# Performance work log

Hardware: AMD Instinct MI355X
Metric: run time of the kernel (lower is better)

Reference implementation:

```python
import jax, jax.numpy as jnp
import numpy as np

N_NODES = 50000
N_EDGES = 800000
N_GRAPHS = 2048


def setup_inputs() -> dict:
    key = jax.random.key(0)
    ks = jax.random.split(key, 16)
    x = jax.random.normal(ks[0], (N_NODES, 32), dtype=jnp.float32)
    edge_index = jax.random.randint(ks[1], (2, N_EDGES), 0, N_NODES, dtype=jnp.int64)
    batch = jnp.sort(jax.random.randint(ks[2], (N_NODES,), 0, N_GRAPHS, dtype=jnp.int64))
    def w(k, fi, fo):
        return jax.random.normal(k, (fi, fo), dtype=jnp.float32) * (1.0 / np.sqrt(fi))
    return {
        "x": x, "edge_index": edge_index, "batch": batch,
        "W1": w(ks[3], 32, 64), "b1": jnp.zeros((64,), jnp.float32),
        "W2": w(ks[4], 64, 64), "b2": jnp.zeros((64,), jnp.float32),
        "W3": w(ks[5], 64, 64), "b3": jnp.zeros((64,), jnp.float32),
        "lw1": w(ks[6], 64, 64), "lb1": jnp.zeros((64,), jnp.float32),
        "lw2": w(ks[7], 64, 2), "lb2": jnp.zeros((2,), jnp.float32),
    }


def reference(x, edge_index, batch, W1, b1, W2, b2, W3, b3, lw1, lb1, lw2, lb2):
    N = x.shape[0]
    # GCNConv default: add self loops, symmetric normalization
    loops = jnp.arange(N, dtype=edge_index.dtype)
    src = jnp.concatenate([edge_index[0], loops])
    dst = jnp.concatenate([edge_index[1], loops])
    ones = jnp.ones_like(src, dtype=x.dtype)
    deg = jax.ops.segment_sum(ones, dst, num_segments=N)  # in-degree incl. self loops
    dinv = jnp.where(deg > 0, jax.lax.rsqrt(deg), 0.0)
    norm = dinv[src] * dinv[dst]  # [E+N]

    def gcn_relu(h, W, b):
        h = h @ W                                    # [N, F]
        msg = h[src] * norm[:, None]                 # gather + scale [E+N, F]
        out = jax.ops.segment_sum(msg, dst, num_segments=N) + b
        return jax.nn.relu(out)

    h = gcn_relu(x, W1, b1)
    h = gcn_relu(h, W2, b2)
    h = gcn_relu(h, W3, b3)

    # global_mean_pool over graph ids
    summed = jax.ops.segment_sum(h, batch, num_segments=N_GRAPHS)  # [G, F]
    counts = jax.ops.segment_sum(jnp.ones((N,), h.dtype), batch, num_segments=N_GRAPHS)
    pooled = summed / jnp.maximum(counts, 1.0)[:, None]

    # dropout is identity in eval mode
    out = jax.nn.relu(pooled @ lw1 + lb1) @ lw2 + lb2
    return out
```

## Files before the change

### kernel.cpp

```cpp
#include <hip/hip_runtime.h>

#define NN 50000
#define NE 800000
#define NG 2048
#define F 64

constexpr int NB = (NN + 255) / 256;

typedef float f4 __attribute__((ext_vector_type(4)));

static __device__ __forceinline__ int ntload_i(const int* p) {
    return __builtin_nontemporal_load(p);
}

__global__ void deg_kernel(const int* __restrict__ dst, int* __restrict__ deg) {
    int e = blockIdx.x * 256 + threadIdx.x;
    if (e < NE) atomicAdd(&deg[ntload_i(&dst[e])], 1);
}

__global__ void scalex_kernel(const int* __restrict__ deg, const float4* __restrict__ x4,
                              float* __restrict__ dinv, float4* __restrict__ xd4) {
    int i = blockIdx.x * 256 + threadIdx.x;
    if (i < NN * 8) {
        int v = i >> 3;
        float d = rsqrtf((float)(deg[v] + 1));
        if ((i & 7) == 0) dinv[v] = d;
        float4 a = x4[i];
        a.x *= d; a.y *= d; a.z *= d; a.w *= d;
        xd4[i] = a;
    }
}

__global__ void scan1_kernel(const int* __restrict__ deg, int* __restrict__ bsums) {
    __shared__ int s[256];
    int t = threadIdx.x, i = blockIdx.x * 256 + t;
    s[t] = (i < NN) ? deg[i] : 0;
    __syncthreads();
    for (int off = 128; off > 0; off >>= 1) {
        if (t < off) s[t] += s[t + off];
        __syncthreads();
    }
    if (t == 0) bsums[blockIdx.x] = s[0];
}

__global__ void scan23_kernel(const int* __restrict__ deg, const int* __restrict__ bsums,
                              int* __restrict__ rowptr, int* __restrict__ cursor) {
    __shared__ int offs[256];
    __shared__ int s[256];
    int t = threadIdx.x, blk = blockIdx.x;
    offs[t] = (t < NB) ? bsums[t] : 0;
    __syncthreads();
    for (int o = 1; o < 256; o <<= 1) {
        int x = (t >= o) ? offs[t - o] : 0;
        __syncthreads();
        offs[t] += x;
        __syncthreads();
    }
    int chunk_off = (blk > 0) ? offs[blk - 1] : 0;
    int i = blk * 256 + t;
    int v = (i < NN) ? deg[i] : 0;
    s[t] = v;
    __syncthreads();
    for (int o = 1; o < 256; o <<= 1) {
        int x = (t >= o) ? s[t - o] : 0;
        __syncthreads();
        s[t] += x;
        __syncthreads();
    }
    if (i < NN) {
        int rp = chunk_off + s[t] - v;
        rowptr[i] = rp;
        cursor[i] = rp;
    }
    if (blk == 0 && t == 0) rowptr[NN] = NE;
}

__global__ void fill_kernel(const int* __restrict__ src, const int* __restrict__ dst,
                            int* __restrict__ cursor, unsigned short* __restrict__ col) {
    int e = blockIdx.x * 256 + threadIdx.x;
    if (e < NE) {
        int sv = ntload_i(&src[e]);
        int slot = atomicAdd(&cursor[ntload_i(&dst[e])], 1);
        col[slot] = (unsigned short)sv;
    }
}

__global__ void agg32_kernel(const f4* __restrict__ g4, const int* __restrict__ rowptr,
                             const unsigned short* __restrict__ col, const float* __restrict__ dinv,
                             float* __restrict__ out) {
    int lane = threadIdx.x & 63;
    int v = blockIdx.x * 4 + (threadIdx.x >> 6);
    int slot = lane >> 3, fq = lane & 7;
    int beg = rowptr[v], end = rowptr[v + 1];
    f4 acc = {0.f, 0.f, 0.f, 0.f};
    for (int base = beg; base < end; base += 32) {
        f4 a[4];
        float w[4];
#pragma unroll
        for (int j = 0; j < 4; ++j) {
            int e = base + slot + j * 8;
            int ce = (e < end) ? e : (end - 1);
            w[j] = (e < end) ? 1.f : 0.f;
            int u = col[ce];
            a[j] = g4[(long)u * 8 + fq];
        }
#pragma unroll
        for (int j = 0; j < 4; ++j) acc += w[j] * a[j];
    }
#pragma unroll
    for (int m = 8; m < 64; m <<= 1) {
        acc.x += __shfl_xor(acc.x, m);
        acc.y += __shfl_xor(acc.y, m);
        acc.z += __shfl_xor(acc.z, m);
        acc.w += __shfl_xor(acc.w, m);
    }
    f4 self = g4[(long)v * 8 + fq];
    float d = dinv[v];
    acc = d * (acc + self);
    if (slot < 4) {
        float comp = (slot == 0) ? acc.x : (slot == 1) ? acc.y : (slot == 2) ? acc.z : acc.w;
        out[(long)v * 32 + 4 * fq + slot] = comp;
    }
}

template <bool POOL>
__global__ void agg4h_kernel(const f4* __restrict__ g, const int* __restrict__ rowptr,
                             const unsigned short* __restrict__ col, const float* __restrict__ dinv,
                             const f4* __restrict__ bias4, float* __restrict__ out,
                             const int* __restrict__ batch, float* __restrict__ pooled,
                             float* __restrict__ counts) {
    int tid = threadIdx.x, lane = tid & 63, w = tid >> 6;
    int bi = blockIdx.x;
    int h = (bi & 7) >> 2;
    int idx = ((bi >> 3) << 2) | (bi & 3);
    int base = idx * 64 + w * 16;
    if (base >= NN) return;
    int slot = lane >> 3, fq = lane & 7;
    const f4* gb = g + (long)h * NN * 8;
    int li = base + ((lane < 17) ? lane : 16);
    if (li > NN) li = NN;
    int rpv = rowptr[li];
#pragma unroll 1
    for (int i = 0; i < 16; ++i) {
        int v = base + i;
        if (v >= NN) break;
        int beg = __shfl(rpv, i), end = __shfl(rpv, i + 1);
        f4 acc = {0.f, 0.f, 0.f, 0.f};
        for (int b0 = beg; b0 < end; b0 += 32) {
            f4 a[4];
            float wt[4];
#pragma unroll
            for (int j = 0; j < 4; ++j) {
                int e = b0 + slot + j * 8;
                int ce = (e < end) ? e : (end - 1);
                wt[j] = (e < end) ? 1.f : 0.f;
                int u = col[ce];
                a[j] = gb[(long)u * 8 + fq];
            }
#pragma unroll
            for (int j = 0; j < 4; ++j) acc += wt[j] * a[j];
        }
#pragma unroll
        for (int m = 8; m < 64; m <<= 1) {
            acc.x += __shfl_xor(acc.x, m);
            acc.y += __shfl_xor(acc.y, m);
            acc.z += __shfl_xor(acc.z, m);
            acc.w += __shfl_xor(acc.w, m);
        }
        f4 self = gb[(long)v * 8 + fq];
        float d = dinv[v];
        f4 bb = bias4[h * 8 + fq];
        f4 hv;
        hv.x = fmaxf(fmaf(d, acc.x + self.x, bb.x), 0.f);
        hv.y = fmaxf(fmaf(d, acc.y + self.y, bb.y), 0.f);
        hv.z = fmaxf(fmaf(d, acc.z + self.z, bb.z), 0.f);
        hv.w = fmaxf(fmaf(d, acc.w + self.w, bb.w), 0.f);
        if (slot < 4) {
            float comp = (slot == 0) ? hv.x : (slot == 1) ? hv.y : (slot == 2) ? hv.z : hv.w;
            int feat = h * 32 + fq * 4 + slot;
            if (POOL) {
                atomicAdd(&pooled[(long)batch[v] * F + feat], comp);
            } else {
                out[(long)v * F + feat] = comp;
            }
        }
        if (POOL && h == 0 && lane == 0) atomicAdd(&counts[batch[v]], 1.0f);
    }
}

template <int K, bool RELU_BIAS>
__global__ void gemm_kernel(const float* __restrict__ in, const float* __restrict__ W,
                            const float* __restrict__ bias, const float* __restrict__ dinv,
                            float* __restrict__ out) {
    __shared__ float Ws[K * F];
    int t = threadIdx.x;
#pragma unroll
    for (int i = 0; i < K * F / 256; ++i) Ws[i * 256 + t] = W[i * 256 + t];
    __syncthreads();
    int f = t & 63;
    int slot = __builtin_amdgcn_readfirstlane(t >> 6);
    int n0 = blockIdx.x * 16 + slot;
    float acc0 = 0.f, acc1 = 0.f, acc2 = 0.f, acc3 = 0.f;
    const float* r0 = in + (long)n0 * K;
    const float* r1 = r0 + 4 * K;
    const float* r2 = r0 + 8 * K;
    const float* r3 = r0 + 12 * K;
#pragma unroll
    for (int k = 0; k < K; ++k) {
        float w = Ws[k * F + f];
        acc0 = fmaf(r0[k], w, acc0);
        acc1 = fmaf(r1[k], w, acc1);
        acc2 = fmaf(r2[k], w, acc2);
        acc3 = fmaf(r3[k], w, acc3);
    }
    if (RELU_BIAS) {
        float b = bias[f];
        out[(long)n0 * F + f]        = fmaxf(acc0 + b, 0.f);
        out[(long)(n0 + 4) * F + f]  = fmaxf(acc1 + b, 0.f);
        out[(long)(n0 + 8) * F + f]  = fmaxf(acc2 + b, 0.f);
        out[(long)(n0 + 12) * F + f] = fmaxf(acc3 + b, 0.f);
    } else {
        int hh = f >> 5, fl = f & 31;
        float* o = out + (long)hh * NN * 32 + fl;
        o[(long)n0 * 32]        = dinv[n0] * acc0;
        o[(long)(n0 + 4) * 32]  = dinv[n0 + 4] * acc1;
        o[(long)(n0 + 8) * 32]  = dinv[n0 + 8] * acc2;
        o[(long)(n0 + 12) * 32] = dinv[n0 + 12] * acc3;
    }
}

__global__ void head_kernel(const float* __restrict__ pooled, const float* __restrict__ counts,
                            const float* __restrict__ lw1, const float* __restrict__ lb1,
                            const float* __restrict__ lw2, const float* __restrict__ lb2,
                            float* __restrict__ out) {
    __shared__ float p[F];
    __shared__ float hid[F];
    int gid = blockIdx.x, t = threadIdx.x;
    float cnt = fmaxf(counts[gid], 1.0f);
    p[t] = pooled[(long)gid * F + t] / cnt;
    __syncthreads();
    float acc = lb1[t];
#pragma unroll 8
    for (int k = 0; k < F; ++k) acc = fmaf(p[k], lw1[k * F + t], acc);
    hid[t] = fmaxf(acc, 0.f);
    __syncthreads();
    if (t < 2) {
        float a = lb2[t];
#pragma unroll 8
        for (int k = 0; k < F; ++k) a = fmaf(hid[k], lw2[k * 2 + t], a);
        out[(long)gid * 2 + t] = a;
    }
}

extern "C" void kernel_launch(void* const* d_in, const int* in_sizes, int n_in,
                              void* d_out, int out_size, void* d_ws, size_t ws_size,
                              hipStream_t stream) {
    const float* x    = (const float*)d_in[0];
    const int*   ei   = (const int*)d_in[1];
    const int*   bat  = (const int*)d_in[2];
    const float* W1   = (const float*)d_in[3];
    const float* b1   = (const float*)d_in[4];
    const float* W2   = (const float*)d_in[5];
    const float* b2   = (const float*)d_in[6];
    const float* W3   = (const float*)d_in[7];
    const float* b3   = (const float*)d_in[8];
    const float* lw1  = (const float*)d_in[9];
    const float* lb1  = (const float*)d_in[10];
    const float* lw2  = (const float*)d_in[11];
    const float* lb2  = (const float*)d_in[12];
    float* out = (float*)d_out;

    const int* src = ei;
    const int* dst = ei + NE;

    char* ws = (char*)d_ws;
    size_t off = 0;
    auto carve = [&](size_t bytes) {
        void* p = ws + off;
        off += (bytes + 255) & ~(size_t)255;
        return p;
    };
    int*   deg     = (int*)carve(NN * 4);
    float* dinv    = (float*)carve(NN * 4);
    int*   rowptr  = (int*)carve((NN + 1) * 4);
    int*   cursor  = (int*)carve(NN * 4);
    int*   bsums   = (int*)carve(256 * 4);
    unsigned short* col = (unsigned short*)carve((size_t)NE * 2);
    float* xd      = (float*)carve((size_t)NN * 32 * 4);
    float* sbuf    = (float*)carve((size_t)NN * 32 * 4);
    float* bufA    = (float*)carve((size_t)NN * F * 4);
    float* bufB    = (float*)carve((size_t)NN * F * 4);
    float* pooled  = (float*)carve((size_t)NG * F * 4 + NG * 4);
    float* counts  = pooled + (size_t)NG * F;

    hipMemsetAsync(deg, 0, NN * 4, stream);
    hipMemsetAsync(pooled, 0, ((size_t)NG * F + NG) * 4, stream);

    deg_kernel<<<(NE + 255) / 256, 256, 0, stream>>>(dst, deg);
    scalex_kernel<<<(NN * 8 + 255) / 256, 256, 0, stream>>>(deg, (const float4*)x, dinv, (float4*)xd);
    scan1_kernel<<<NB, 256, 0, stream>>>(deg, bsums);
    scan23_kernel<<<NB, 256, 0, stream>>>(deg, bsums, rowptr, cursor);
    fill_kernel<<<(NE + 255) / 256, 256, 0, stream>>>(src, dst, cursor, col);

    const int gridN = NN / 4;
    const int gridH = 196 * 8;
    const int gridG = NN / 16;

    agg32_kernel<<<gridN, 256, 0, stream>>>((const f4*)xd, rowptr, col, dinv, sbuf);
    gemm_kernel<32, true><<<gridG, 256, 0, stream>>>(sbuf, W1, b1, dinv, bufA);

    gemm_kernel<64, false><<<gridG, 256, 0, stream>>>(bufA, W2, nullptr, dinv, bufB);
    agg4h_kernel<false><<<gridH, 256, 0, stream>>>((const f4*)bufB, rowptr, col, dinv,
                                                   (const f4*)b2, bufA,
                                                   nullptr, nullptr, nullptr);
    gemm_kernel<64, false><<<gridG, 256, 0, stream>>>(bufA, W3, nullptr, dinv, bufB);
    agg4h_kernel<true><<<gridH, 256, 0, stream>>>((const f4*)bufB, rowptr, col, dinv,
                                                  (const f4*)b3, nullptr,
                                                  bat, pooled, counts);
    head_kernel<<<NG, 64, 0, stream>>>(pooled, counts, lw1, lb1, lw2, lb2, out);
}
```

Measured before the change: 304.3 us.

## Split aggregation features into 16-wide column slabs for narrower gathers

The GEMM output and the scaled input features are now stored as separate slabs of 16 features per node (four slabs for 64 features, two for 32). Each aggregation block handles one slab, so a gathered neighbour row is 64 bytes and 16 edges are processed in parallel per wave. The layer-1 aggregation also moves to the slab layout with blocked node ranges. The aim is a smaller per-slab working set that fits better in cache and more edge-level parallelism per node. The cost is more blocks, more passes over the CSR indices, and shorter 64-byte gather segments.

```diff
diff --git a/kernel.cpp b/kernel.cpp
--- a/kernel.cpp
+++ b/kernel.cpp
@@ -18,16 +18,16 @@
     if (e < NE) atomicAdd(&deg[ntload_i(&dst[e])], 1);
 }
 
-__global__ void scalex_kernel(const int* __restrict__ deg, const float4* __restrict__ x4,
-                              float* __restrict__ dinv, float4* __restrict__ xd4) {
+__global__ void scalex_kernel(const int* __restrict__ deg, const f4* __restrict__ x4,
+                              float* __restrict__ dinv, f4* __restrict__ xdh) {
     int i = blockIdx.x * 256 + threadIdx.x;
     if (i < NN * 8) {
-        int v = i >> 3;
+        int v = i >> 3, ff = i & 7;
         float d = rsqrtf((float)(deg[v] + 1));
-        if ((i & 7) == 0) dinv[v] = d;
-        float4 a = x4[i];
-        a.x *= d; a.y *= d; a.z *= d; a.w *= d;
-        xd4[i] = a;
+        if (ff == 0) dinv[v] = d;
+        f4 a = x4[i];
+        int h = ff >> 2, fj = ff & 3;
+        xdh[((long)h * NN + v) * 4 + fj] = d * a;
     }
 }
 
@@ -85,58 +85,17 @@
     }
 }
 
-__global__ void agg32_kernel(const f4* __restrict__ g4, const int* __restrict__ rowptr,
-                             const unsigned short* __restrict__ col, const float* __restrict__ dinv,
-                             float* __restrict__ out) {
-    int lane = threadIdx.x & 63;
-    int v = blockIdx.x * 4 + (threadIdx.x >> 6);
-    int slot = lane >> 3, fq = lane & 7;
-    int beg = rowptr[v], end = rowptr[v + 1];
-    f4 acc = {0.f, 0.f, 0.f, 0.f};
-    for (int base = beg; base < end; base += 32) {
-        f4 a[4];
-        float w[4];
-#pragma unroll
-        for (int j = 0; j < 4; ++j) {
-            int e = base + slot + j * 8;
-            int ce = (e < end) ? e : (end - 1);
-            w[j] = (e < end) ? 1.f : 0.f;
-            int u = col[ce];
-            a[j] = g4[(long)u * 8 + fq];
-        }
-#pragma unroll
-        for (int j = 0; j < 4; ++j) acc += w[j] * a[j];
-    }
-#pragma unroll
-    for (int m = 8; m < 64; m <<= 1) {
-        acc.x += __shfl_xor(acc.x, m);
-        acc.y += __shfl_xor(acc.y, m);
-        acc.z += __shfl_xor(acc.z, m);
-        acc.w += __shfl_xor(acc.w, m);
-    }
-    f4 self = g4[(long)v * 8 + fq];
-    float d = dinv[v];
-    acc = d * (acc + self);
-    if (slot < 4) {
-        float comp = (slot == 0) ? acc.x : (slot == 1) ? acc.y : (slot == 2) ? acc.z : acc.w;
-        out[(long)v * 32 + 4 * fq + slot] = comp;
-    }
-}
-
-template <bool POOL>
-__global__ void agg4h_kernel(const f4* __restrict__ g, const int* __restrict__ rowptr,
-                             const unsigned short* __restrict__ col, const float* __restrict__ dinv,
-                             const f4* __restrict__ bias4, float* __restrict__ out,
-                             const int* __restrict__ batch, float* __restrict__ pooled,
-                             float* __restrict__ counts) {
+__global__ void agg32h_kernel(const f4* __restrict__ xdh, const int* __restrict__ rowptr,
+                              const unsigned short* __restrict__ col, const float* __restrict__ dinv,
+                              float* __restrict__ out) {
     int tid = threadIdx.x, lane = tid & 63, w = tid >> 6;
     int bi = blockIdx.x;
     int h = (bi & 7) >> 2;
-    int idx = ((bi >> 3) << 2) | (bi & 3);
-    int base = idx * 64 + w * 16;
+    int sub = ((bi >> 3) << 2) | (bi & 3);
+    int base = sub * 64 + w * 16;
     if (base >= NN) return;
-    int slot = lane >> 3, fq = lane & 7;
-    const f4* gb = g + (long)h * NN * 8;
+    int slot = lane >> 2, fj = lane & 3;
+    const f4* gb = xdh + (long)h * NN * 4;
     int li = base + ((lane < 17) ? lane : 16);
     if (li > NN) li = NN;
     int rpv = rowptr[li];
@@ -147,29 +106,81 @@
         int beg = __shfl(rpv, i), end = __shfl(rpv, i + 1);
         f4 acc = {0.f, 0.f, 0.f, 0.f};
         for (int b0 = beg; b0 < end; b0 += 32) {
-            f4 a[4];
-            float wt[4];
-#pragma unroll
-            for (int j = 0; j < 4; ++j) {
-                int e = b0 + slot + j * 8;
+            f4 a[2];
+            float wt[2];
+#pragma unroll
+            for (int j = 0; j < 2; ++j) {
+                int e = b0 + slot + j * 16;
                 int ce = (e < end) ? e : (end - 1);
                 wt[j] = (e < end) ? 1.f : 0.f;
                 int u = col[ce];
-                a[j] = gb[(long)u * 8 + fq];
+                a[j] = gb[(long)u * 4 + fj];
             }
-#pragma unroll
-            for (int j = 0; j < 4; ++j) acc += wt[j] * a[j];
-        }
-#pragma unroll
-        for (int m = 8; m < 64; m <<= 1) {
+            acc += wt[0] * a[0] + wt[1] * a[1];
+        }
+#pragma unroll
+        for (int m = 4; m < 64; m <<= 1) {
             acc.x += __shfl_xor(acc.x, m);
             acc.y += __shfl_xor(acc.y, m);
             acc.z += __shfl_xor(acc.z, m);
             acc.w += __shfl_xor(acc.w, m);
         }
-        f4 self = gb[(long)v * 8 + fq];
+        f4 self = gb[(long)v * 4 + fj];
         float d = dinv[v];
-        f4 bb = bias4[h * 8 + fq];
+        acc = d * (acc + self);
+        if (slot < 4) {
+            float comp = (slot == 0) ? acc.x : (slot == 1) ? acc.y : (slot == 2) ? acc.z : acc.w;
+            out[(long)v * 32 + h * 16 + fj * 4 + slot] = comp;
+        }
+    }
+}
+
+template <bool POOL>
+__global__ void agg4q_kernel(const f4* __restrict__ gq, const int* __restrict__ rowptr,
+                             const unsigned short* __restrict__ col, const float* __restrict__ dinv,
+                             const f4* __restrict__ bias4, float* __restrict__ out,
+                             const int* __restrict__ batch, float* __restrict__ pooled,
+                             float* __restrict__ counts) {
+    int tid = threadIdx.x, lane = tid & 63, w = tid >> 6;
+    int bi = blockIdx.x;
+    int q = (bi & 7) >> 1;
+    int sub = ((bi >> 3) << 1) | (bi & 1);
+    int base = sub * 64 + w * 16;
+    if (base >= NN) return;
+    int slot = lane >> 2, fj = lane & 3;
+    const f4* gb = gq + (long)q * NN * 4;
+    int li = base + ((lane < 17) ? lane : 16);
+    if (li > NN) li = NN;
+    int rpv = rowptr[li];
+#pragma unroll 1
+    for (int i = 0; i < 16; ++i) {
+        int v = base + i;
+        if (v >= NN) break;
+        int beg = __shfl(rpv, i), end = __shfl(rpv, i + 1);
+        f4 acc = {0.f, 0.f, 0.f, 0.f};
+        for (int b0 = beg; b0 < end; b0 += 32) {
+            f4 a[2];
+            float wt[2];
+#pragma unroll
+            for (int j = 0; j < 2; ++j) {
+                int e = b0 + slot + j * 16;
+                int ce = (e < end) ? e : (end - 1);
+                wt[j] = (e < end) ? 1.f : 0.f;
+                int u = col[ce];
+                a[j] = gb[(long)u * 4 + fj];
+            }
+            acc += wt[0] * a[0] + wt[1] * a[1];
+        }
+#pragma unroll
+        for (int m = 4; m < 64; m <<= 1) {
+            acc.x += __shfl_xor(acc.x, m);
+            acc.y += __shfl_xor(acc.y, m);
+            acc.z += __shfl_xor(acc.z, m);
+            acc.w += __shfl_xor(acc.w, m);
+        }
+        f4 self = gb[(long)v * 4 + fj];
+        float d = dinv[v];
+        f4 bb = bias4[q * 4 + fj];
         f4 hv;
         hv.x = fmaxf(fmaf(d, acc.x + self.x, bb.x), 0.f);
         hv.y = fmaxf(fmaf(d, acc.y + self.y, bb.y), 0.f);
@@ -177,14 +188,14 @@
         hv.w = fmaxf(fmaf(d, acc.w + self.w, bb.w), 0.f);
         if (slot < 4) {
             float comp = (slot == 0) ? hv.x : (slot == 1) ? hv.y : (slot == 2) ? hv.z : hv.w;
-            int feat = h * 32 + fq * 4 + slot;
+            int feat = q * 16 + fj * 4 + slot;
             if (POOL) {
                 atomicAdd(&pooled[(long)batch[v] * F + feat], comp);
             } else {
                 out[(long)v * F + feat] = comp;
             }
         }
-        if (POOL && h == 0 && lane == 0) atomicAdd(&counts[batch[v]], 1.0f);
+        if (POOL && q == 0 && lane == 0) atomicAdd(&counts[batch[v]], 1.0f);
     }
 }
 
@@ -220,12 +231,12 @@
         out[(long)(n0 + 8) * F + f]  = fmaxf(acc2 + b, 0.f);
         out[(long)(n0 + 12) * F + f] = fmaxf(acc3 + b, 0.f);
     } else {
-        int hh = f >> 5, fl = f & 31;
-        float* o = out + (long)hh * NN * 32 + fl;
-        o[(long)n0 * 32]        = dinv[n0] * acc0;
-        o[(long)(n0 + 4) * 32]  = dinv[n0 + 4] * acc1;
-        o[(long)(n0 + 8) * 32]  = dinv[n0 + 8] * acc2;
-        o[(long)(n0 + 12) * 32] = dinv[n0 + 12] * acc3;
+        int q = f >> 4, fl = f & 15;
+        float* o = out + (long)q * NN * 16 + fl;
+        o[(long)n0 * 16]        = dinv[n0] * acc0;
+        o[(long)(n0 + 4) * 16]  = dinv[n0 + 4] * acc1;
+        o[(long)(n0 + 8) * 16]  = dinv[n0 + 8] * acc2;
+        o[(long)(n0 + 12) * 16] = dinv[n0 + 12] * acc3;
     }
 }
 
@@ -297,24 +308,24 @@
     hipMemsetAsync(pooled, 0, ((size_t)NG * F + NG) * 4, stream);
 
     deg_kernel<<<(NE + 255) / 256, 256, 0, stream>>>(dst, deg);
-    scalex_kernel<<<(NN * 8 + 255) / 256, 256, 0, stream>>>(deg, (const float4*)x, dinv, (float4*)xd);
+    scalex_kernel<<<(NN * 8 + 255) / 256, 256, 0, stream>>>(deg, (const f4*)x, dinv, (f4*)xd);
     scan1_kernel<<<NB, 256, 0, stream>>>(deg, bsums);
     scan23_kernel<<<NB, 256, 0, stream>>>(deg, bsums, rowptr, cursor);
     fill_kernel<<<(NE + 255) / 256, 256, 0, stream>>>(src, dst, cursor, col);
 
-    const int gridN = NN / 4;
-    const int gridH = 196 * 8;
+    const int gridH = 8 * 196;
+    const int gridQ = 8 * 392;
     const int gridG = NN / 16;
 
-    agg32_kernel<<<gridN, 256, 0, stream>>>((const f4*)xd, rowptr, col, dinv, sbuf);
+    agg32h_kernel<<<gridH, 256, 0, stream>>>((const f4*)xd, rowptr, col, dinv, sbuf);
     gemm_kernel<32, true><<<gridG, 256, 0, stream>>>(sbuf, W1, b1, dinv, bufA);
 
     gemm_kernel<64, false><<<gridG, 256, 0, stream>>>(bufA, W2, nullptr, dinv, bufB);
-    agg4h_kernel<false><<<gridH, 256, 0, stream>>>((const f4*)bufB, rowptr, col, dinv,
+    agg4q_kernel<false><<<gridQ, 256, 0, stream>>>((const f4*)bufB, rowptr, col, dinv,
                                                    (const f4*)b2, bufA,
                                                    nullptr, nullptr, nullptr);
     gemm_kernel<64, false><<<gridG, 256, 0, stream>>>(bufA, W3, nullptr, dinv, bufB);
-    agg4h_kernel<true><<<gridH, 256, 0, stream>>>((const f4*)bufB, rowptr, col, dinv,
+    agg4q_kernel<true><<<gridQ, 256, 0, stream>>>((const f4*)bufB, rowptr, col, dinv,
                                                   (const f4*)b3, nullptr,
                                                   bat, pooled, counts);
     head_kernel<<<NG, 64, 0, stream>>>(pooled, counts, lw1, lb1, lw2, lb2, out);
```

New measurement: 363.9 us. +19.6%, slower.
